# Kernel tuning notes

Hardware: AMD Instinct MI355X
Metric: run time of the kernel (lower is better)

## Reference

```python
import jax, jax.numpy as jnp
import numpy as np

EPS = 1e-5
K = 7        # deformable/spatial kernel size
GRID = 4     # local pool grid size


def conv(x, w, pad=0):
    # x: NCHW, w: OIHW
    return jax.lax.conv_general_dilated(
        x, w, (1, 1), [(pad, pad), (pad, pad)],
        dimension_numbers=('NCHW', 'OIHW', 'NCHW'))


def bn(x, g, b, m, v):
    # eval-mode batchnorm with running stats
    scale = (g * jax.lax.rsqrt(v + EPS))[None, :, None, None]
    return (x - m[None, :, None, None]) * scale + b[None, :, None, None]


def grid_sample(feat, grid):
    # bilinear, padding_mode='zeros', align_corners=False
    # feat: [b,c,h,w], grid: [b,h,w,2] with (x,y) in [-1,1]
    b, c, h, w = feat.shape
    gx = (grid[..., 0] + 1.0) * (w * 0.5) - 0.5
    gy = (grid[..., 1] + 1.0) * (h * 0.5) - 0.5
    x0 = jnp.floor(gx)
    y0 = jnp.floor(gy)
    wx = gx - x0
    wy = gy - y0
    feat_flat = feat.reshape(b, c, h * w)

    def gather(yi, xi):
        valid = (xi >= 0) & (xi < w) & (yi >= 0) & (yi < h)
        xi_c = jnp.clip(xi, 0, w - 1).astype(jnp.int32)
        yi_c = jnp.clip(yi, 0, h - 1).astype(jnp.int32)
        idx = (yi_c * w + xi_c).reshape(b, 1, h * w)
        vals = jnp.take_along_axis(feat_flat, idx, axis=2).reshape(b, c, h, w)
        return vals * valid[:, None].astype(feat.dtype)

    out = (gather(y0, x0) * ((1 - wx) * (1 - wy))[:, None]
           + gather(y0, x0 + 1) * (wx * (1 - wy))[:, None]
           + gather(y0 + 1, x0) * ((1 - wx) * wy)[:, None]
           + gather(y0 + 1, x0 + 1) * (wx * wy)[:, None])
    return out


def cmife_forward(x, align_w, align_g, align_b, align_m, align_v,
                  mlp_w1, mlp_w2, loc_w1, loc_w2, fusion_w,
                  off_w1, off_g, off_bt, off_m, off_v, off_w2, off_b2,
                  attn_w):
    # ---- align: 1x1 conv + BN + SiLU ----
    x = conv(x, align_w)
    x = bn(x, align_g, align_b, align_m, align_v)
    x = x * jax.nn.sigmoid(x)  # SiLU
    b_, c_, h_, w_ = x.shape

    # ---- LocalGlobalChannelAttention ----
    def mlp(z):
        return conv(jax.nn.relu(conv(z, mlp_w1)), mlp_w2)

    g_avg = mlp(jnp.mean(x, (2, 3), keepdims=True))
    g_max = mlp(jnp.max(x, (2, 3), keepdims=True))
    global_attn = g_avg + g_max
    # adaptive avg pool to GRIDxGRID (h,w divisible by GRID)
    loc = x.reshape(b_, c_, GRID, h_ // GRID, GRID, w_ // GRID).mean((3, 5))
    local_attn = conv(jax.nn.relu(conv(loc, loc_w1)), loc_w2)
    local_attn = local_attn.mean((2, 3), keepdims=True)
    alpha = jax.nn.sigmoid(fusion_w)
    ca = jax.nn.sigmoid(alpha * global_attn + (1 - alpha) * local_attn)
    x = ca * x

    # ---- DeformableSpatialAttention ----
    avg_out = jnp.mean(x, 1, keepdims=True)
    max_out = jnp.max(x, 1, keepdims=True)
    sf = jnp.concatenate([avg_out, max_out], axis=1)  # [b,2,h,w]
    o = jax.nn.relu(bn(conv(sf, off_w1, pad=1), off_g, off_bt, off_m, off_v))
    o = conv(o, off_w2, pad=1) + off_b2[None, :, None, None]  # [b,2*K*K,h,w]
    off = o.reshape(b_, 2, K * K, h_, w_).mean(2)             # [b,2,h,w]
    off = jnp.tanh(off) * 0.5
    off = jnp.transpose(off, (0, 2, 3, 1))                    # [b,h,w,2]
    gy, gx = jnp.meshgrid(jnp.linspace(-1.0, 1.0, h_),
                          jnp.linspace(-1.0, 1.0, w_), indexing='ij')
    base = jnp.stack([gx, gy], axis=-1)[None]                 # [1,h,w,2]
    dgrid = jnp.clip(base + off, -1.0, 1.0)
    sampled = grid_sample(sf, dgrid)                          # [b,2,h,w]
    sa = jax.nn.sigmoid(conv(sampled, attn_w, pad=K // 2))    # [b,1,h,w]
    return sa * x


def setup_inputs() -> dict:
    key = jax.random.key(0)
    ks = jax.random.split(key, 24)
    B, CIN, COUT, H, W, MID = 8, 256, 256, 160, 160, 16
    f = jnp.float32
    inp = {
        'x': jax.random.normal(ks[0], (B, CIN, H, W), f),
        'align_w': jax.random.normal(ks[1], (COUT, CIN, 1, 1), f) * 0.05,
        'align_g': jax.random.uniform(ks[2], (COUT,), f, 0.5, 1.5),
        'align_b': jax.random.normal(ks[3], (COUT,), f) * 0.1,
        'align_m': jax.random.normal(ks[4], (COUT,), f) * 0.1,
        'align_v': jax.random.uniform(ks[5], (COUT,), f, 0.5, 1.5),
        'mlp_w1': jax.random.normal(ks[6], (MID, COUT, 1, 1), f) * 0.1,
        'mlp_w2': jax.random.normal(ks[7], (COUT, MID, 1, 1), f) * 0.1,
        'loc_w1': jax.random.normal(ks[8], (MID, COUT, 1, 1), f) * 0.1,
        'loc_w2': jax.random.normal(ks[9], (COUT, MID, 1, 1), f) * 0.1,
        'fusion_w': jnp.float32(0.5),
        'off_w1': jax.random.normal(ks[10], (16, 2, 3, 3), f) * 0.1,
        'off_g': jax.random.uniform(ks[11], (16,), f, 0.5, 1.5),
        'off_bt': jax.random.normal(ks[12], (16,), f) * 0.1,
        'off_m': jax.random.normal(ks[13], (16,), f) * 0.1,
        'off_v': jax.random.uniform(ks[14], (16,), f, 0.5, 1.5),
        'off_w2': jax.random.normal(ks[15], (2 * K * K, 16, 3, 3), f) * 0.01,
        'off_b2': jax.random.normal(ks[16], (2 * K * K,), f) * 0.01,
        'attn_w': jax.random.normal(ks[17], (1, 2, K, K), f) * 0.1,
    }
    return inp


def reference(x, align_w, align_g, align_b, align_m, align_v,
              mlp_w1, mlp_w2, loc_w1, loc_w2, fusion_w,
              off_w1, off_g, off_bt, off_m, off_v, off_w2, off_b2,
              attn_w):
    return cmife_forward(x, align_w, align_g, align_b, align_m, align_v,
                         mlp_w1, mlp_w2, loc_w1, loc_w2, fusion_w,
                         off_w1, off_g, off_bt, off_m, off_v, off_w2, off_b2,
                         attn_w)
```

## Files before the change

### kernel.cpp

```cpp
#include <hip/hip_runtime.h>
#include <hip/hip_bf16.h>

#define HH 160
#define WW 160
#define HW 25600
#define NC 256
#define NB 8

typedef short short8 __attribute__((ext_vector_type(8)));
typedef float f32x4 __attribute__((ext_vector_type(4)));

__device__ __forceinline__ unsigned short f2bf(float f) {
    unsigned u = __float_as_uint(f);
    u += 0x7fffu + ((u >> 16) & 1u);
    return (unsigned short)(u >> 16);
}
__device__ __forceinline__ float bf2f(unsigned short h) {
    return __uint_as_float(((unsigned)h) << 16);
}

__global__ void k0_fold(const float* __restrict__ aw, const float* __restrict__ ag,
                        const float* __restrict__ ab, const float* __restrict__ am,
                        const float* __restrict__ av,
                        unsigned short* __restrict__ wpkh, unsigned short* __restrict__ wpkl,
                        float* __restrict__ biasp) {
    int co = blockIdx.x, t = threadIdx.x;
    float sc = ag[co] * rsqrtf(av[co] + 1e-5f);
    float w = aw[co * 256 + t] * sc;
    unsigned short h = f2bf(w);
    int kk = t >> 5, kq = t & 31;
    wpkh[kk * 10240 + co * 40 + kq] = h;
    wpkl[kk * 10240 + co * 40 + kq] = f2bf(w - bf2f(h));
    if (t == 0) biasp[co] = ab[co] - am[co] * sc;
}

__global__ void k0b_fold2(const float* __restrict__ ow2, const float* __restrict__ ob2,
                          float* __restrict__ weff, float* __restrict__ beff) {
    int t = threadIdx.x;
    if (t < 288) {
        int g = t / 144, r = t - g * 144;
        float s = 0.f;
        for (int q = 0; q < 49; q++) s += ow2[(size_t)(g * 49 + q) * 144 + r];
        weff[t] = s * (1.f / 49.f);
    }
    if (t < 2) {
        float s = 0.f;
        for (int q = 0; q < 49; q++) s += ob2[t * 49 + q];
        beff[t] = s * (1.f / 49.f);
    }
}

__global__ __launch_bounds__(256, 2) void k1_gemm(
    const float* __restrict__ X, const unsigned short* __restrict__ Wph,
    const unsigned short* __restrict__ Wpl,
    const float* __restrict__ biasp, float* __restrict__ xal) {
    __shared__ __align__(16) unsigned short Ah[10240];
    __shared__ __align__(16) unsigned short Al[10240];
    __shared__ __align__(16) unsigned short Bh[5120];
    __shared__ __align__(16) unsigned short Bl[5120];

    int t = threadIdx.x;
    int n0 = blockIdx.x * 128;
    int b  = blockIdx.y;
    const float* Xb = X + (size_t)b * NC * HW;

    int lane = t & 63, wv = t >> 6;
    int lcol = lane & 15, lq = lane >> 4;

    f32x4 acc[4][8];
#pragma unroll
    for (int i = 0; i < 4; i++)
#pragma unroll
        for (int j = 0; j < 8; j++) { f32x4 z = {0.f, 0.f, 0.f, 0.f}; acc[i][j] = z; }

    int bn2 = t & 63;
    int bkq = t >> 6;

    for (int kk = 0; kk < 8; kk++) {
        const char* gah = (const char*)(Wph + kk * 10240);
        const char* gal = (const char*)(Wpl + kk * 10240);
#pragma unroll
        for (int i = 0; i < 5; i++) {
            int off = wv * 1024 + i * 4096;
            __builtin_amdgcn_global_load_lds(
                (const __attribute__((address_space(1))) unsigned int*)(gah + off + lane * 16),
                (__attribute__((address_space(3))) unsigned int*)((char*)Ah + off),
                16, 0, 0);
            __builtin_amdgcn_global_load_lds(
                (const __attribute__((address_space(1))) unsigned int*)(gal + off + lane * 16),
                (__attribute__((address_space(3))) unsigned int*)((char*)Al + off),
                16, 0, 0);
        }
#pragma unroll
        for (int j2 = 0; j2 < 2; j2++) {
            int kq = bkq + 4 * j2;
            const float* src = Xb + (size_t)(kk * 32 + kq * 4) * HW + n0 + bn2 * 2;
            unsigned h0[2], h1[2], l0[2], l1[2];
#pragma unroll
            for (int j = 0; j < 2; j++) {
                float2 v0 = *(const float2*)(src + (size_t)(2 * j) * HW);
                float2 v1 = *(const float2*)(src + (size_t)(2 * j + 1) * HW);
                unsigned short a = f2bf(v0.x), bq = f2bf(v1.x);
                unsigned short c = f2bf(v0.y), d = f2bf(v1.y);
                h0[j] = (unsigned)a | ((unsigned)bq << 16);
                h1[j] = (unsigned)c | ((unsigned)d << 16);
                unsigned short la = f2bf(v0.x - bf2f(a)), lb = f2bf(v1.x - bf2f(bq));
                unsigned short lc = f2bf(v0.y - bf2f(c)), ld = f2bf(v1.y - bf2f(d));
                l0[j] = (unsigned)la | ((unsigned)lb << 16);
                l1[j] = (unsigned)lc | ((unsigned)ld << 16);
            }
            *(uint2*)(&Bh[(bn2 * 2) * 40 + kq * 4])     = make_uint2(h0[0], h0[1]);
            *(uint2*)(&Bh[(bn2 * 2 + 1) * 40 + kq * 4]) = make_uint2(h1[0], h1[1]);
            *(uint2*)(&Bl[(bn2 * 2) * 40 + kq * 4])     = make_uint2(l0[0], l0[1]);
            *(uint2*)(&Bl[(bn2 * 2 + 1) * 40 + kq * 4]) = make_uint2(l1[0], l1[1]);
        }
        __syncthreads();

        short8 afh[4], afl[4];
#pragma unroll
        for (int mt = 0; mt < 4; mt++) {
            afh[mt] = *(const short8*)(&Ah[(wv * 64 + mt * 16 + lcol) * 40 + lq * 8]);
            afl[mt] = *(const short8*)(&Al[(wv * 64 + mt * 16 + lcol) * 40 + lq * 8]);
        }
#pragma unroll
        for (int nt = 0; nt < 8; nt++) {
            short8 bh = *(const short8*)(&Bh[(nt * 16 + lcol) * 40 + lq * 8]);
            short8 bl = *(const short8*)(&Bl[(nt * 16 + lcol) * 40 + lq * 8]);
#pragma unroll
            for (int mt = 0; mt < 4; mt++) {
                acc[mt][nt] = __builtin_amdgcn_mfma_f32_16x16x32_bf16(
                    afh[mt], bh, acc[mt][nt], 0, 0, 0);
                acc[mt][nt] = __builtin_amdgcn_mfma_f32_16x16x32_bf16(
                    afh[mt], bl, acc[mt][nt], 0, 0, 0);
                acc[mt][nt] = __builtin_amdgcn_mfma_f32_16x16x32_bf16(
                    afl[mt], bh, acc[mt][nt], 0, 0, 0);
            }
        }
        __syncthreads();
    }
#pragma unroll
    for (int mt = 0; mt < 4; mt++) {
#pragma unroll
        for (int r = 0; r < 4; r++) {
            int co = wv * 64 + mt * 16 + lq * 4 + r;
            float bias = biasp[co];
            size_t rowbase = ((size_t)b * NC + co) * HW + n0;
#pragma unroll
            for (int nt = 0; nt < 8; nt++) {
                int n = nt * 16 + lcol;
                float y = acc[mt][nt][r] + bias;
                float z = y / (1.f + __expf(-y));
                xal[rowbase + n] = z;
            }
        }
    }
}

__global__ void ka_stats(const float* __restrict__ xal,
                         float* __restrict__ cellsum, float* __restrict__ cellmax) {
    __shared__ float redS[256], redM[256];
    int bc = blockIdx.x;
    int t = threadIdx.x;
    int cell = t >> 4, s = t & 15;
    int ch = cell >> 2, cw = cell & 3;
    const float* base = xal + (size_t)bc * HW;
    float sm = 0.f, mx = -3.4e38f;
    for (int k = 0; k < 100; k++) {
        int idx = s + 16 * k;
        int r = idx / 40, col = idx - r * 40;
        float v = base[(ch * 40 + r) * 160 + cw * 40 + col];
        sm += v;
        mx = fmaxf(mx, v);
    }
    redS[t] = sm;
    redM[t] = mx;
    __syncthreads();
    if (s == 0) {
        float cs = 0.f, cm = -3.4e38f;
#pragma unroll
        for (int i = 0; i < 16; i++) {
            cs += redS[t + i];
            cm = fmaxf(cm, redM[t + i]);
        }
        cellsum[bc * 16 + cell] = cs;
        cellmax[bc * 16 + cell] = cm;
    }
}

__global__ void kb_attn(const float* __restrict__ cellsum, const float* __restrict__ cellmax,
                        const float* __restrict__ mw1, const float* __restrict__ mw2,
                        const float* __restrict__ lw1, const float* __restrict__ lw2,
                        const float* __restrict__ fw, float* __restrict__ ca) {
    __shared__ float avgS[256], maxS[256], locS[256 * 16], hid[32], hlS[256];
    int b = blockIdx.x, t = threadIdx.x;
    float s = 0.f, m = -3.4e38f;
#pragma unroll
    for (int cell = 0; cell < 16; cell++) {
        float cs = cellsum[(b * 256 + t) * 16 + cell];
        float cm = cellmax[(b * 256 + t) * 16 + cell];
        s += cs;
        m = fmaxf(m, cm);
        locS[t * 16 + cell] = cs * (1.f / 1600.f);
    }
    avgS[t] = s * (1.f / 25600.f);
    maxS[t] = m;
    __syncthreads();
    if (t < 32) {
        int j = t & 15;
        const float* w1 = mw1 + j * 256;
        const float* src = (t < 16) ? avgS : maxS;
        float h = 0.f;
        for (int c = 0; c < 256; c++) h += w1[c] * src[c];
        hid[t] = fmaxf(h, 0.f);
    }
    {
        int cell = t >> 4, j = t & 15;
        const float* w1 = lw1 + j * 256;
        float h = 0.f;
        for (int c = 0; c < 256; c++) h += w1[c] * locS[c * 16 + cell];
        hlS[t] = fmaxf(h, 0.f);
    }
    __syncthreads();
    float ga = 0.f, gm = 0.f;
#pragma unroll
    for (int j = 0; j < 16; j++) {
        float w2 = mw2[t * 16 + j];
        ga += w2 * hid[j];
        gm += w2 * hid[16 + j];
    }
    float la = 0.f;
#pragma unroll
    for (int cell = 0; cell < 16; cell++)
#pragma unroll
        for (int j = 0; j < 16; j++)
            la += lw2[t * 16 + j] * hlS[cell * 16 + j];
    float alpha = 1.f / (1.f + expf(-fw[0]));
    float pre = alpha * (ga + gm) + (1.f - alpha) * (la * (1.f / 16.f));
    ca[b * 256 + t] = 1.f / (1.f + expf(-pre));
}

__global__ void k3_sf(const float* __restrict__ xal,
                      const float* __restrict__ ca, float* __restrict__ sf) {
    __shared__ float cas[256];
    int b = blockIdx.y, t = threadIdx.x;
    cas[t] = ca[b * 256 + t];
    __syncthreads();
    int p = blockIdx.x * 256 + t;
    const float* base = xal + (size_t)b * NC * HW + p;
    float s0 = 0.f, m0 = -3.4e38f;
    for (int c = 0; c < 256; c++) {
        float a0 = cas[c] * base[(size_t)c * HW];
        s0 += a0;
        m0 = fmaxf(m0, a0);
    }
    sf[(size_t)b * 2 * HW + p]      = s0 * (1.f / 256.f);
    sf[(size_t)b * 2 * HW + HW + p] = m0;
}

__global__ void k4_conv1(const float* __restrict__ sf, const float* __restrict__ ow1,
                         const float* __restrict__ og, const float* __restrict__ obt,
                         const float* __restrict__ om, const float* __restrict__ ov,
                         float* __restrict__ o1) {
    __shared__ float wS[288], scS[16], shS[16];
    int b = blockIdx.y, t = threadIdx.x;
    for (int i = t; i < 288; i += 256) wS[i] = ow1[i];
    if (t < 16) {
        float sc = og[t] * rsqrtf(ov[t] + 1e-5f);
        scS[t] = sc;
        shS[t] = obt[t] - om[t] * sc;
    }
    __syncthreads();
    int p = blockIdx.x * 256 + t;
    int h = p / 160, w = p - h * 160;
    const float* a0 = sf + (size_t)b * 2 * HW;
    const float* a1 = a0 + HW;
    float in0[9], in1[9];
#pragma unroll
    for (int kh = 0; kh < 3; kh++)
#pragma unroll
        for (int kw = 0; kw < 3; kw++) {
            int hh = h + kh - 1, ww = w + kw - 1;
            bool ok = (hh >= 0) & (hh < 160) & (ww >= 0) & (ww < 160);
            int q = hh * 160 + ww;
            in0[kh * 3 + kw] = ok ? a0[q] : 0.f;
            in1[kh * 3 + kw] = ok ? a1[q] : 0.f;
        }
    float* outb = o1 + (size_t)b * 16 * HW + p;
#pragma unroll
    for (int j = 0; j < 16; j++) {
        float acc = 0.f;
#pragma unroll
        for (int k = 0; k < 9; k++)
            acc += wS[j * 18 + k] * in0[k] + wS[j * 18 + 9 + k] * in1[k];
        outb[(size_t)j * HW] = fmaxf(acc * scS[j] + shS[j], 0.f);
    }
}

__global__ void k5_sample(const float* __restrict__ o1, const float* __restrict__ weff,
                          const float* __restrict__ beff, const float* __restrict__ sf,
                          float* __restrict__ sampled) {
    __shared__ float tileS[16 * 18 * 18];
    __shared__ float wS[288];
    __shared__ float bS[2];
    int b = blockIdx.y, t = threadIdx.x;
    int ty0 = (blockIdx.x / 10) * 16, tx0 = (blockIdx.x % 10) * 16;
    const float* ob = o1 + (size_t)b * 16 * HW;
    for (int i = t; i < 288; i += 256) wS[i] = weff[i];
    if (t < 2) bS[t] = beff[t];
    for (int i = t; i < 16 * 18 * 18; i += 256) {
        int ci = i / 324, rem = i - ci * 324;
        int r = rem / 18, c = rem - r * 18;
        int gr = ty0 + r - 1, gc = tx0 + c - 1;
        bool ok = (gr >= 0) & (gr < 160) & (gc >= 0) & (gc < 160);
        tileS[i] = ok ? ob[(size_t)ci * HW + gr * 160 + gc] : 0.f;
    }
    __syncthreads();
    int ty = t >> 4, tx = t & 15;
    int h = ty0 + ty, w = tx0 + tx;
    int p = h * 160 + w;
    float s0 = bS[0], s1 = bS[1];
#pragma unroll
    for (int ci = 0; ci < 16; ci++) {
        const float* tb = &tileS[ci * 324 + ty * 18 + tx];
        const float* w0 = &wS[ci * 9];
        const float* w1 = &wS[144 + ci * 9];
#pragma unroll
        for (int kh = 0; kh < 3; kh++)
#pragma unroll
            for (int kw = 0; kw < 3; kw++) {
                float v = tb[kh * 18 + kw];
                s0 += w0[kh * 3 + kw] * v;
                s1 += w1[kh * 3 + kw] * v;
            }
    }
    float ox = tanhf(s0) * 0.5f;
    float oy = tanhf(s1) * 0.5f;
    float bx = w * (2.f / 159.f) - 1.f, by = h * (2.f / 159.f) - 1.f;
    float gxn = fminf(fmaxf(bx + ox, -1.f), 1.f);
    float gyn = fminf(fmaxf(by + oy, -1.f), 1.f);
    float gx = (gxn + 1.f) * 80.f - 0.5f;
    float gy = (gyn + 1.f) * 80.f - 0.5f;
    float x0f = floorf(gx), y0f = floorf(gy);
    float wx = gx - x0f, wy = gy - y0f;
    int ix0 = (int)x0f, iy0 = (int)y0f;
    const float* f0 = sf + (size_t)b * 2 * HW;
    const float* f1 = f0 + HW;
    float r0 = 0.f, r1 = 0.f;
#pragma unroll
    for (int dy = 0; dy < 2; dy++)
#pragma unroll
        for (int dx = 0; dx < 2; dx++) {
            int xi = ix0 + dx, yi = iy0 + dy;
            float wgt = (dx ? wx : 1.f - wx) * (dy ? wy : 1.f - wy);
            if ((xi >= 0) & (xi < 160) & (yi >= 0) & (yi < 160)) {
                int q = yi * 160 + xi;
                r0 += wgt * f0[q];
                r1 += wgt * f1[q];
            }
        }
    float* sb = sampled + (size_t)b * 2 * HW + p;
    sb[0] = r0;
    sb[HW] = r1;
}

__global__ void k5b_sa(const float* __restrict__ sampled, const float* __restrict__ attn_w,
                       float* __restrict__ sa) {
    __shared__ float wS[98];
    int b = blockIdx.y, t = threadIdx.x;
    if (t < 98) wS[t] = attn_w[t];
    __syncthreads();
    int p = blockIdx.x * 256 + t;
    int h = p / 160, w = p - h * 160;
    const float* s0 = sampled + (size_t)b * 2 * HW;
    const float* s1 = s0 + HW;
    float acc = 0.f;
#pragma unroll
    for (int kh = 0; kh < 7; kh++) {
        int hh = h + kh - 3;
        if (hh < 0 || hh >= 160) continue;
#pragma unroll
        for (int kw = 0; kw < 7; kw++) {
            int ww = w + kw - 3;
            if (ww < 0 || ww >= 160) continue;
            int q = hh * 160 + ww;
            acc += wS[kh * 7 + kw] * s0[q] + wS[49 + kh * 7 + kw] * s1[q];
        }
    }
    sa[(size_t)b * HW + p] = 1.f / (1.f + expf(-acc));
}

__global__ void k6_out(float* __restrict__ out, const float* __restrict__ ca,
                       const float* __restrict__ sa) {
    unsigned e4 = blockIdx.x * 256 + threadIdx.x;
    unsigned e = e4 * 4;
    unsigned b = e / (256u * HW);
    unsigned rem = e - b * (256u * HW);
    unsigned c = rem / HW;
    unsigned p = rem - c * HW;
    f32x4 v = *(f32x4*)(out + e);
    f32x4 s = *(const f32x4*)(sa + (size_t)b * HW + p);
    float cav = ca[b * 256 + c];
#pragma unroll
    for (int i = 0; i < 4; i++) v[i] = cav * s[i] * v[i];
    *(f32x4*)(out + e) = v;
}

extern "C" void kernel_launch(void* const* d_in, const int* in_sizes, int n_in,
                              void* d_out, int out_size, void* d_ws, size_t ws_size,
                              hipStream_t stream) {
    const float* x       = (const float*)d_in[0];
    const float* align_w = (const float*)d_in[1];
    const float* align_g = (const float*)d_in[2];
    const float* align_b = (const float*)d_in[3];
    const float* align_m = (const float*)d_in[4];
    const float* align_v = (const float*)d_in[5];
    const float* mlp_w1  = (const float*)d_in[6];
    const float* mlp_w2  = (const float*)d_in[7];
    const float* loc_w1  = (const float*)d_in[8];
    const float* loc_w2  = (const float*)d_in[9];
    const float* fusion  = (const float*)d_in[10];
    const float* off_w1  = (const float*)d_in[11];
    const float* off_g   = (const float*)d_in[12];
    const float* off_bt  = (const float*)d_in[13];
    const float* off_m   = (const float*)d_in[14];
    const float* off_v   = (const float*)d_in[15];
    const float* off_w2  = (const float*)d_in[16];
    const float* off_b2  = (const float*)d_in[17];
    const float* attn_w  = (const float*)d_in[18];
    float* out = (float*)d_out;

    char* wsb = (char*)d_ws;
    size_t off = 0;
    auto alloc = [&](size_t bytes) -> void* {
        off = (off + 255) & ~(size_t)255;
        void* p = wsb + off;
        off += bytes;
        return p;
    };
    float* xal = out;
    unsigned short* wph = (unsigned short*)alloc(81920 * 2);
    unsigned short* wpl = (unsigned short*)alloc(81920 * 2);
    float* biasp   = (float*)alloc(256 * 4);
    float* cellsum = (float*)alloc(32768 * 4);
    float* cellmax = (float*)alloc(32768 * 4);
    float* ca      = (float*)alloc(2048 * 4);
    float* sf      = (float*)alloc((size_t)NB * 2 * HW * 4);
    float* o1      = (float*)alloc((size_t)NB * 16 * HW * 4);
    float* sampled = (float*)alloc((size_t)NB * 2 * HW * 4);
    float* sa      = (float*)alloc((size_t)NB * HW * 4);
    float* weff    = (float*)alloc(288 * 4);
    float* beff    = (float*)alloc(2 * 4);
    (void)ws_size; (void)in_sizes; (void)n_in; (void)out_size;

    k0_fold<<<dim3(256), 256, 0, stream>>>(align_w, align_g, align_b, align_m, align_v,
                                           wph, wpl, biasp);
    k0b_fold2<<<dim3(1), 320, 0, stream>>>(off_w2, off_b2, weff, beff);
    k1_gemm<<<dim3(200, 8), 256, 0, stream>>>(x, wph, wpl, biasp, xal);
    ka_stats<<<dim3(2048), 256, 0, stream>>>(xal, cellsum, cellmax);
    kb_attn<<<dim3(8), 256, 0, stream>>>(cellsum, cellmax, mlp_w1, mlp_w2,
                                         loc_w1, loc_w2, fusion, ca);
    k3_sf<<<dim3(100, 8), 256, 0, stream>>>(xal, ca, sf);
    k4_conv1<<<dim3(100, 8), 256, 0, stream>>>(sf, off_w1, off_g, off_bt, off_m, off_v, o1);
    k5_sample<<<dim3(100, 8), 256, 0, stream>>>(o1, weff, beff, sf, sampled);
    k5b_sa<<<dim3(100, 8), 256, 0, stream>>>(sampled, attn_w, sa);
    k6_out<<<dim3(51200), 256, 0, stream>>>(out, ca, sa);
}
```

Before: 676.4 us.

## Prefetch GEMM tiles across iterations and coalesce cell-statistics reduction

The 1x1-conv GEMM now loads the next K-slice of activations into registers while the current slice is being multiplied. It also issues the async global-to-LDS weight loads for the next slice right after a raw barrier, so memory latency overlaps with MFMA work instead of being serialized. The cell-statistics kernel is rewritten to read contiguous rows with coalesced accesses and to spread the work over four times as many blocks, reducing with per-column accumulators, LDS and wavefront shuffles. The cost is higher register pressure from the prefetch buffers and reliance on correct wait and barrier ordering around the async LDS loads.

```diff
diff --git a/kernel.cpp b/kernel.cpp
--- a/kernel.cpp
+++ b/kernel.cpp
@@ -76,9 +76,21 @@
     int bn2 = t & 63;
     int bkq = t >> 6;
 
-    for (int kk = 0; kk < 8; kk++) {
-        const char* gah = (const char*)(Wph + kk * 10240);
-        const char* gal = (const char*)(Wpl + kk * 10240);
+    float2 pf[8];
+
+#pragma unroll
+    for (int j2 = 0; j2 < 2; j2++) {
+        int kq = bkq + 4 * j2;
+        const float* src = Xb + (size_t)(kq * 4) * HW + n0 + bn2 * 2;
+#pragma unroll
+        for (int j = 0; j < 2; j++) {
+            pf[j2 * 4 + 2 * j]     = *(const float2*)(src + (size_t)(2 * j) * HW);
+            pf[j2 * 4 + 2 * j + 1] = *(const float2*)(src + (size_t)(2 * j + 1) * HW);
+        }
+    }
+    {
+        const char* gah = (const char*)Wph;
+        const char* gal = (const char*)Wpl;
 #pragma unroll
         for (int i = 0; i < 5; i++) {
             int off = wv * 1024 + i * 4096;
@@ -91,15 +103,17 @@
                 (__attribute__((address_space(3))) unsigned int*)((char*)Al + off),
                 16, 0, 0);
         }
+    }
+
+    for (int kk = 0; kk < 8; kk++) {
 #pragma unroll
         for (int j2 = 0; j2 < 2; j2++) {
             int kq = bkq + 4 * j2;
-            const float* src = Xb + (size_t)(kk * 32 + kq * 4) * HW + n0 + bn2 * 2;
             unsigned h0[2], h1[2], l0[2], l1[2];
 #pragma unroll
             for (int j = 0; j < 2; j++) {
-                float2 v0 = *(const float2*)(src + (size_t)(2 * j) * HW);
-                float2 v1 = *(const float2*)(src + (size_t)(2 * j + 1) * HW);
+                float2 v0 = pf[j2 * 4 + 2 * j];
+                float2 v1 = pf[j2 * 4 + 2 * j + 1];
                 unsigned short a = f2bf(v0.x), bq = f2bf(v1.x);
                 unsigned short c = f2bf(v0.y), d = f2bf(v1.y);
                 h0[j] = (unsigned)a | ((unsigned)bq << 16);
@@ -122,6 +136,18 @@
             afh[mt] = *(const short8*)(&Ah[(wv * 64 + mt * 16 + lcol) * 40 + lq * 8]);
             afl[mt] = *(const short8*)(&Al[(wv * 64 + mt * 16 + lcol) * 40 + lq * 8]);
         }
+        if (kk < 7) {
+#pragma unroll
+            for (int j2 = 0; j2 < 2; j2++) {
+                int kq = bkq + 4 * j2;
+                const float* src = Xb + (size_t)((kk + 1) * 32 + kq * 4) * HW + n0 + bn2 * 2;
+#pragma unroll
+                for (int j = 0; j < 2; j++) {
+                    pf[j2 * 4 + 2 * j]     = *(const float2*)(src + (size_t)(2 * j) * HW);
+                    pf[j2 * 4 + 2 * j + 1] = *(const float2*)(src + (size_t)(2 * j + 1) * HW);
+                }
+            }
+        }
 #pragma unroll
         for (int nt = 0; nt < 8; nt++) {
             short8 bh = *(const short8*)(&Bh[(nt * 16 + lcol) * 40 + lq * 8]);
@@ -136,7 +162,23 @@
                     afl[mt], bh, acc[mt][nt], 0, 0, 0);
             }
         }
-        __syncthreads();
+        asm volatile("s_barrier" ::: "memory");
+        if (kk < 7) {
+            const char* gah = (const char*)(Wph + (kk + 1) * 10240);
+            const char* gal = (const char*)(Wpl + (kk + 1) * 10240);
+#pragma unroll
+            for (int i = 0; i < 5; i++) {
+                int off = wv * 1024 + i * 4096;
+                __builtin_amdgcn_global_load_lds(
+                    (const __attribute__((address_space(1))) unsigned int*)(gah + off + lane * 16),
+                    (__attribute__((address_space(3))) unsigned int*)((char*)Ah + off),
+                    16, 0, 0);
+                __builtin_amdgcn_global_load_lds(
+                    (const __attribute__((address_space(1))) unsigned int*)(gal + off + lane * 16),
+                    (__attribute__((address_space(3))) unsigned int*)((char*)Al + off),
+                    16, 0, 0);
+            }
+        }
     }
 #pragma unroll
     for (int mt = 0; mt < 4; mt++) {
@@ -158,32 +200,42 @@
 
 __global__ void ka_stats(const float* __restrict__ xal,
                          float* __restrict__ cellsum, float* __restrict__ cellmax) {
-    __shared__ float redS[256], redM[256];
-    int bc = blockIdx.x;
+    __shared__ float rs[4][256], rm[4][256];
+    int blk = blockIdx.x;
+    int bc = blk >> 2, ch = blk & 3;
+    const float* base = xal + (size_t)bc * HW + ch * 6400;
     int t = threadIdx.x;
-    int cell = t >> 4, s = t & 15;
-    int ch = cell >> 2, cw = cell & 3;
-    const float* base = xal + (size_t)bc * HW;
-    float sm = 0.f, mx = -3.4e38f;
-    for (int k = 0; k < 100; k++) {
-        int idx = s + 16 * k;
-        int r = idx / 40, col = idx - r * 40;
-        float v = base[(ch * 40 + r) * 160 + cw * 40 + col];
-        sm += v;
-        mx = fmaxf(mx, v);
-    }
-    redS[t] = sm;
-    redM[t] = mx;
-    __syncthreads();
-    if (s == 0) {
-        float cs = 0.f, cm = -3.4e38f;
-#pragma unroll
-        for (int i = 0; i < 16; i++) {
-            cs += redS[t + i];
-            cm = fmaxf(cm, redM[t + i]);
-        }
-        cellsum[bc * 16 + cell] = cs;
-        cellmax[bc * 16 + cell] = cm;
+    float s0 = 0.f, s1 = 0.f, s2 = 0.f, s3 = 0.f;
+    float m0 = -3.4e38f, m1 = -3.4e38f, m2 = -3.4e38f, m3 = -3.4e38f;
+    int c = (t < 160) ? t : t - 160;
+#pragma unroll 5
+    for (int i = 0; i < 25; i++) {
+        float v = base[i * 256 + t];
+        bool w0 = c < 40;
+        bool w1 = (c >= 40) & (c < 80);
+        bool w2 = (c >= 80) & (c < 120);
+        bool w3 = c >= 120;
+        s0 += w0 ? v : 0.f;  m0 = w0 ? fmaxf(m0, v) : m0;
+        s1 += w1 ? v : 0.f;  m1 = w1 ? fmaxf(m1, v) : m1;
+        s2 += w2 ? v : 0.f;  m2 = w2 ? fmaxf(m2, v) : m2;
+        s3 += w3 ? v : 0.f;  m3 = w3 ? fmaxf(m3, v) : m3;
+        c += 96; if (c >= 160) c -= 160;
+    }
+    rs[0][t] = s0; rs[1][t] = s1; rs[2][t] = s2; rs[3][t] = s3;
+    rm[0][t] = m0; rm[1][t] = m1; rm[2][t] = m2; rm[3][t] = m3;
+    __syncthreads();
+    int g = t >> 6, i0 = t & 63;
+    float sv = rs[g][i0] + rs[g][i0 + 64] + rs[g][i0 + 128] + rs[g][i0 + 192];
+    float mv = fmaxf(fmaxf(rm[g][i0], rm[g][i0 + 64]),
+                     fmaxf(rm[g][i0 + 128], rm[g][i0 + 192]));
+#pragma unroll
+    for (int off = 32; off >= 1; off >>= 1) {
+        sv += __shfl_down(sv, off, 64);
+        mv = fmaxf(mv, __shfl_down(mv, off, 64));
+    }
+    if (i0 == 0) {
+        cellsum[bc * 16 + ch * 4 + g] = sv;
+        cellmax[bc * 16 + ch * 4 + g] = mv;
     }
 }
 
@@ -456,7 +508,7 @@
                                            wph, wpl, biasp);
     k0b_fold2<<<dim3(1), 320, 0, stream>>>(off_w2, off_b2, weff, beff);
     k1_gemm<<<dim3(200, 8), 256, 0, stream>>>(x, wph, wpl, biasp, xal);
-    ka_stats<<<dim3(2048), 256, 0, stream>>>(xal, cellsum, cellmax);
+    ka_stats<<<dim3(8192), 256, 0, stream>>>(xal, cellsum, cellmax);
     kb_attn<<<dim3(8), 256, 0, stream>>>(cellsum, cellmax, mlp_w1, mlp_w2,
                                          loc_w1, loc_w2, fusion, ca);
     k3_sf<<<dim3(100, 8), 256, 0, stream>>>(xal, ca, sf);
```

Result: no change. 682.0 us (+0.8%).
